# Optimization experiments

Measured on AMD Instinct MI355X. Metric: run time of the kernel, lower is better.

Reference implementation:

```python
import jax, jax.numpy as jnp
import numpy as np

DIM = 256; SEQ = 2048; WIN = 64; HEADS = 4; RANK = 32; LAYERS = 3; VOCAB = 32000
EPS = 1e-6

def _unit(v):
    # unit_normalize_values: project onto unit sphere along feature dim
    return v / jnp.maximum(jnp.linalg.norm(v, axis=-1, keepdims=True), EPS)

def _signed_softmax(s):
    # signed_softmax_state: sign(s) * softmax(|s|) over nodes
    return jnp.sign(s) * jax.nn.softmax(jnp.abs(s), axis=-1)

def setup_inputs() -> dict:
    key = jax.random.key(0)
    ks = jax.random.split(key, 10)
    d = DIM
    return {
        "input_ids": jax.random.randint(ks[0], (2, SEQ), 0, VOCAB, dtype=jnp.int32),
        "emb": 0.02 * jax.random.normal(ks[1], (VOCAB, d), jnp.float32),
        "pos_emb": 0.02 * jax.random.normal(ks[2], (SEQ, d), jnp.float32),
        "anchor_val": 0.02 * jax.random.normal(ks[3], (d,), jnp.float32),
        "anchor_state": jnp.zeros((), jnp.float32),
        "Ws": 0.02 * jax.random.normal(ks[4], (d,), jnp.float32),
        "bs": jnp.zeros((), jnp.float32),
        "U": 0.02 * jax.random.normal(ks[5], (LAYERS, d, HEADS, RANK), jnp.float32),
        "V": 0.02 * jax.random.normal(ks[6], (LAYERS, d, HEADS, RANK), jnp.float32),
        "W1": 0.02 * jax.random.normal(ks[7], (LAYERS, d, 2 * d), jnp.float32),
        "b1": jnp.zeros((LAYERS, 2 * d), jnp.float32),
        "W2": 0.02 * jax.random.normal(ks[8], (LAYERS, 2 * d, d), jnp.float32),
        "b2": jnp.zeros((LAYERS, d), jnp.float32),
    }

def _forward(emb, pos_emb, anchor_val, anchor_state, Ws, bs, U, V, W1, b1, W2, b2, input_ids):
    B, S = input_ids.shape
    tok = emb[input_ids] + pos_emb[None, :S]          # [B,S,D]
    state_src = tok                                    # state projected from pre-unit-norm values
    tok = _unit(tok)
    tstate = state_src @ Ws + bs                       # [B,S] scalar state per node
    val = jnp.concatenate([jnp.broadcast_to(_unit(anchor_val), (B, 1, DIM)), tok], axis=1)
    state = jnp.concatenate([jnp.broadcast_to(anchor_state, (B, 1)), tstate], axis=1)
    N = S + 1
    offs = jnp.arange(-WIN, WIN + 1)
    idx = jnp.arange(N)[:, None] + offs[None, :]       # [N,K]
    valid = (idx >= 0) & (idx < N)
    idxc = jnp.clip(idx, 0, N - 1)
    inv_sqrt_r = np.float32(1.0 / np.sqrt(RANK))
    for l in range(LAYERS):
        q = jnp.einsum('bnd,dhr->bnhr', val, U[l])
        k = jnp.einsum('bnd,dhr->bnhr', val, V[l])
        knb = k[:, idxc]                               # [B,N,K,H,R] window gather
        s = jnp.einsum('bnhr,bnkhr->bnkh', q, knb) * inv_sqrt_r
        s = s.max(axis=-1)                             # max head-aggregate [B,N,K]
        a = jnp.where(valid, jnp.abs(s), -jnp.inf)
        wgt = jnp.where(valid, jnp.sign(s) * jax.nn.softmax(a, axis=-1), 0.0)  # signed-abs-softmax edges
        dval = jnp.einsum('bnk,bnkd->bnd', wgt, val[:, idxc])
        dstate = jnp.sum(wgt * state[:, idxc], axis=-1)
        # apply_delta: residual + norm(identity) + unit-norm + touched-mask where
        updated = val + dval
        nv = _unit(updated)
        touched = jnp.max(jnp.abs(jax.lax.stop_gradient(dval)), axis=-1, keepdims=True) > 0
        val = jnp.where(touched, nv, updated)
        state = _signed_softmax(state + dstate)
        # residual feed-forward then re-unit-norm
        h = jax.nn.gelu(jnp.einsum('bnd,dh->bnh', val, W1[l]) + b1[l], approximate=False)
        val = _unit(val + jnp.einsum('bnh,hd->bnd', h, W2[l]) + b2[l])
    return state, val

def reference(input_ids, emb, pos_emb, anchor_val, anchor_state, Ws, bs, U, V, W1, b1, W2, b2):
    return _forward(emb, pos_emb, anchor_val, anchor_state, Ws, bs, U, V, W1, b1, W2, b2, input_ids)
```

## Files before the change

### kernel.cpp

```cpp
#include <hip/hip_runtime.h>
#include <hip/hip_bf16.h>
#include <math.h>

#define BB 2
#define SS 2048
#define NN 2049
#define MM (BB*NN)
#define DD 256
#define HR 128
#define NHEAD 4
#define WINW 64
#define DFF 512
#define EPSF 1e-6f
#define TB8 257

typedef __attribute__((ext_vector_type(8))) short bf16x8;
typedef __attribute__((ext_vector_type(4))) float f32x4;

__device__ __forceinline__ float wave_sum(float v) {
    v += __shfl_down(v, 32, 64); v += __shfl_down(v, 16, 64);
    v += __shfl_down(v, 8, 64);  v += __shfl_down(v, 4, 64);
    v += __shfl_down(v, 2, 64);  v += __shfl_down(v, 1, 64);
    return v;
}
__device__ __forceinline__ float wave_max(float v) {
    v = fmaxf(v, __shfl_down(v, 32, 64)); v = fmaxf(v, __shfl_down(v, 16, 64));
    v = fmaxf(v, __shfl_down(v, 8, 64));  v = fmaxf(v, __shfl_down(v, 4, 64));
    v = fmaxf(v, __shfl_down(v, 2, 64));  v = fmaxf(v, __shfl_down(v, 1, 64));
    return v;
}
__device__ __forceinline__ float block_sum(float v, float* red) {
    v = wave_sum(v);
    __syncthreads();
    if ((threadIdx.x & 63) == 0) red[threadIdx.x >> 6] = v;
    __syncthreads();
    return red[0] + red[1] + red[2] + red[3];
}
__device__ __forceinline__ float sgnf(float x) {
    return (x > 0.f) ? 1.f : ((x < 0.f) ? -1.f : 0.f);
}
__device__ __forceinline__ ushort f2b(float x) {
    __hip_bfloat16 h = __float2bfloat16(x);
    return *(ushort*)&h;
}
__device__ __forceinline__ float b2f(ushort u) {
    unsigned int v = ((unsigned int)u) << 16;
    return *(float*)&v;
}
__device__ __forceinline__ void split3(float x, ushort& h, ushort& m, ushort& l) {
    h = f2b(x);
    float r1 = x - b2f(h);
    m = f2b(r1);
    l = f2b(r1 - b2f(m));
}
__device__ __forceinline__ void pack_map(int e, int N, int& k, int& n) {
    int j = e & 7;
    int l = (e >> 3) & 63;
    int c = e >> 9;
    int ntiles = N >> 4;
    int kt = c / ntiles, nt = c - kt * ntiles;
    k = kt * 32 + ((l >> 4) << 3) + j;
    n = nt * 16 + (l & 15);
}

__global__ void pre_kernel(const int* __restrict__ ids,
                           const float* __restrict__ emb,
                           const float* __restrict__ pos,
                           const float* __restrict__ anchor_val,
                           const float* __restrict__ anchor_state,
                           const float* __restrict__ Ws,
                           const float* __restrict__ bs,
                           float* __restrict__ val,
                           float* __restrict__ state,
                           const float* __restrict__ W1, const float* __restrict__ W2,
                           const float* __restrict__ U,  const float* __restrict__ V,
                           ushort* __restrict__ W1ph, ushort* __restrict__ W1pl,
                           ushort* __restrict__ W2ph, ushort* __restrict__ W2pl,
                           ushort* __restrict__ U0, ushort* __restrict__ U1,
                           ushort* __restrict__ U2,
                           ushort* __restrict__ V0, ushort* __restrict__ V1,
                           ushort* __restrict__ V2) {
    __shared__ float red[4];
    int bid = blockIdx.x;
    int t = threadIdx.x;
    if (bid < MM) {
        int b = bid / NN, n = bid % NN;
        float e;
        if (n == 0) {
            e = anchor_val[t];
        } else {
            int id = ids[b * SS + (n - 1)];
            e = emb[(size_t)id * DD + t] + pos[(size_t)(n - 1) * DD + t];
        }
        float ss = block_sum(e * e, red);
        float ts = block_sum(e * Ws[t], red);
        float rn = 1.f / fmaxf(sqrtf(ss), EPSF);
        float o = e * rn;
        val[(size_t)bid * DD + t] = o;
        if (t == 0) state[bid] = (n == 0) ? anchor_state[0] : (ts + bs[0]);
        return;
    }
    int idx = (bid - MM) * 256 + t;
    int l = idx / 327680;
    int r = idx - l * 327680;
    if (l >= 3) return;
    int k, n;
    if (r < 131072) {
        int e = r;
        pack_map(e, 512, k, n);
        float s = W1[(size_t)l * 131072 + (size_t)k * 512 + n];
        ushort h = f2b(s);
        W1ph[(size_t)l * 131072 + e] = h;
        W1pl[(size_t)l * 131072 + e] = f2b(s - b2f(h));
    } else if (r < 262144) {
        int e = r - 131072;
        pack_map(e, 256, k, n);
        float s = W2[(size_t)l * 131072 + (size_t)k * 256 + n];
        ushort h = f2b(s);
        W2ph[(size_t)l * 131072 + e] = h;
        W2pl[(size_t)l * 131072 + e] = f2b(s - b2f(h));
    } else if (r < 294912) {
        int e = r - 262144;
        pack_map(e, 128, k, n);
        ushort h, m, lo;
        split3(U[(size_t)l * 32768 + (size_t)k * 128 + n], h, m, lo);
        U0[(size_t)l * 32768 + e] = h;
        U1[(size_t)l * 32768 + e] = m;
        U2[(size_t)l * 32768 + e] = lo;
    } else {
        int e = r - 294912;
        pack_map(e, 128, k, n);
        ushort h, m, lo;
        split3(V[(size_t)l * 32768 + (size_t)k * 128 + n], h, m, lo);
        V0[(size_t)l * 32768 + e] = h;
        V1[(size_t)l * 32768 + e] = m;
        V2[(size_t)l * 32768 + e] = lo;
    }
}

__global__ __launch_bounds__(256, 3)
void proj_kernel(const float* __restrict__ Xin,
                 const ushort* __restrict__ U0, const ushort* __restrict__ U1,
                 const ushort* __restrict__ U2,
                 const ushort* __restrict__ V0, const ushort* __restrict__ V1,
                 const ushort* __restrict__ V2,
                 ushort* __restrict__ q0, ushort* __restrict__ q1,
                 ushort* __restrict__ q2,
                 ushort* __restrict__ k0, ushort* __restrict__ k1,
                 ushort* __restrict__ k2,
                 float* __restrict__ valG, int donorm) {
    __shared__ __align__(16) ushort pln[3][16 * 256];
    int t = threadIdx.x;
    int w = t >> 6, l = t & 63;
    int lm = l & 15, quad = l >> 4;
    int m0 = blockIdx.x * 16;
    bool isQ = (blockIdx.y == 0);
    const ushort* P0 = isQ ? U0 : V0;
    const ushort* P1 = isQ ? U1 : V1;
    const ushort* P2 = isQ ? U2 : V2;

    #pragma unroll
    for (int rr = 0; rr < 4; rr++) {
        int row = w * 4 + rr;
        int tok = m0 + row; if (tok > MM - 1) tok = MM - 1;
        f32x4 x = *(const f32x4*)(Xin + (size_t)tok * DD + l * 4);
        if (donorm) {
            float s = x[0]*x[0] + x[1]*x[1] + x[2]*x[2] + x[3]*x[3];
            #pragma unroll
            for (int off = 1; off < 64; off <<= 1) s += __shfl_xor(s, off, 64);
            float rn = 1.f / fmaxf(sqrtf(s), EPSF);
            x[0] *= rn; x[1] *= rn; x[2] *= rn; x[3] *= rn;
            if (isQ) *(f32x4*)(valG + (size_t)tok * DD + l * 4) = x;
        }
        ushort4 h4, m4, l4;
        ushort hh, mm, ll;
        split3(x[0], hh, mm, ll); h4.x = hh; m4.x = mm; l4.x = ll;
        split3(x[1], hh, mm, ll); h4.y = hh; m4.y = mm; l4.y = ll;
        split3(x[2], hh, mm, ll); h4.z = hh; m4.z = mm; l4.z = ll;
        split3(x[3], hh, mm, ll); h4.w = hh; m4.w = mm; l4.w = ll;
        unsigned byte = ((unsigned)(row * 512 + l * 8)) ^ ((unsigned)((row & 7) << 4));
        *(ushort4*)((char*)&pln[0][0] + byte) = h4;
        *(ushort4*)((char*)&pln[1][0] + byte) = m4;
        *(ushort4*)((char*)&pln[2][0] + byte) = l4;
    }
    __syncthreads();

    f32x4 acc[2];
    acc[0] = (f32x4)(0.f); acc[1] = (f32x4)(0.f);
    #pragma unroll
    for (int kt = 0; kt < 8; kt++) {
        unsigned abyte = ((unsigned)(lm * 512 + kt * 64 + quad * 16)) ^
                         ((unsigned)((lm & 7) << 4));
        bf16x8 a0 = *(const bf16x8*)((char*)&pln[0][0] + abyte);
        bf16x8 a1 = *(const bf16x8*)((char*)&pln[1][0] + abyte);
        bf16x8 a2 = *(const bf16x8*)((char*)&pln[2][0] + abyte);
        #pragma unroll
        for (int jj = 0; jj < 2; jj++) {
            int ntl = w * 2 + jj;
            size_t off = ((size_t)(kt * 8 + ntl) * 64 + l) * 8;
            bf16x8 b0 = *(const bf16x8*)(P0 + off);
            bf16x8 b1 = *(const bf16x8*)(P1 + off);
            bf16x8 b2 = *(const bf16x8*)(P2 + off);
            acc[jj] = __builtin_amdgcn_mfma_f32_16x16x32_bf16(a0, b0, acc[jj], 0, 0, 0);
            acc[jj] = __builtin_amdgcn_mfma_f32_16x16x32_bf16(a0, b1, acc[jj], 0, 0, 0);
            acc[jj] = __builtin_amdgcn_mfma_f32_16x16x32_bf16(a1, b0, acc[jj], 0, 0, 0);
            acc[jj] = __builtin_amdgcn_mfma_f32_16x16x32_bf16(a1, b1, acc[jj], 0, 0, 0);
            acc[jj] = __builtin_amdgcn_mfma_f32_16x16x32_bf16(a0, b2, acc[jj], 0, 0, 0);
            acc[jj] = __builtin_amdgcn_mfma_f32_16x16x32_bf16(a2, b0, acc[jj], 0, 0, 0);
        }
    }
    ushort* o0 = isQ ? q0 : k0;
    ushort* o1 = isQ ? q1 : k1;
    ushort* o2 = isQ ? q2 : k2;
    #pragma unroll
    for (int jj = 0; jj < 2; jj++) {
        int n = (w * 2 + jj) * 16 + lm;
        #pragma unroll
        for (int r = 0; r < 4; r++) {
            int tok = m0 + quad * 4 + r;
            if (tok < MM) {
                ushort h, m, lo;
                split3(acc[jj][r], h, m, lo);
                size_t oi = (size_t)tok * HR + n;
                o0[oi] = h; o1[oi] = m; o2[oi] = lo;
            }
        }
    }
}

__global__ __launch_bounds__(256, 3)
void attn_kernel(const float* __restrict__ val_in,
                 const float* __restrict__ state_in,
                 const ushort* __restrict__ q0, const ushort* __restrict__ q1,
                 const ushort* __restrict__ q2,
                 const ushort* __restrict__ k0, const ushort* __restrict__ k1,
                 const ushort* __restrict__ k2,
                 float* __restrict__ val_out,
                 ushort* __restrict__ vbH, ushort* __restrict__ vbM,
                 float* __restrict__ dstate_out) {
    __shared__ float sc4[NHEAD][8][148];
    __shared__ float wgt2[144][12];
    __shared__ float redS[8][4];
    __shared__ float redM[8][4];

    int b = blockIdx.x / TB8;
    int n0 = (blockIdx.x % TB8) * 8;
    int t = threadIdx.x;
    int w = t >> 6, l = t & 63;
    int lm = l & 15, quad = l >> 4;

    {
        int qrow = n0 + (lm & 7);
        if (qrow > NN - 1) qrow = NN - 1;
        size_t qa = ((size_t)(b * NN + qrow)) * HR + w * 32 + quad * 8;
        bf16x8 a0 = *(const bf16x8*)(q0 + qa);
        bf16x8 a1 = *(const bf16x8*)(q1 + qa);
        bf16x8 a2 = *(const bf16x8*)(q2 + qa);
        #pragma unroll
        for (int jt = 0; jt < 9; jt++) {
            int j = n0 - 64 + jt * 16 + lm;
            j = (j < 0) ? 0 : ((j > NN - 1) ? NN - 1 : j);
            size_t ka = ((size_t)(b * NN + j)) * HR + w * 32 + quad * 8;
            bf16x8 kf0 = *(const bf16x8*)(k0 + ka);
            bf16x8 kf1 = *(const bf16x8*)(k1 + ka);
            bf16x8 kf2 = *(const bf16x8*)(k2 + ka);
            f32x4 acc = (f32x4)(0.f);
            acc = __builtin_amdgcn_mfma_f32_16x16x32_bf16(a0, kf0, acc, 0, 0, 0);
            acc = __builtin_amdgcn_mfma_f32_16x16x32_bf16(a0, kf1, acc, 0, 0, 0);
            acc = __builtin_amdgcn_mfma_f32_16x16x32_bf16(a1, kf0, acc, 0, 0, 0);
            acc = __builtin_amdgcn_mfma_f32_16x16x32_bf16(a1, kf1, acc, 0, 0, 0);
            acc = __builtin_amdgcn_mfma_f32_16x16x32_bf16(a0, kf2, acc, 0, 0, 0);
            acc = __builtin_amdgcn_mfma_f32_16x16x32_bf16(a2, kf0, acc, 0, 0, 0);
            if (quad < 2) {
                #pragma unroll
                for (int r = 0; r < 4; r++)
                    sc4[w][quad * 4 + r][jt * 16 + lm] = acc[r];
            }
        }
    }
    __syncthreads();

    {
        int m = t >> 5, p = t & 31;
        int n = n0 + m;
        bool tokv = (n < NN);
        float sv[5]; bool vv[5];
        float mx = -INFINITY;
        #pragma unroll
        for (int i = 0; i < 5; i++) {
            int tap = p + 32 * i;
            bool inb = (tap < 144);
            int tapc = inb ? tap : 0;
            int j = n0 - 64 + tapc;
            float s0 = sc4[0][m][tapc], s1 = sc4[1][m][tapc];
            float s2 = sc4[2][m][tapc], s3 = sc4[3][m][tapc];
            float s = fmaxf(fmaxf(s0, s1), fmaxf(s2, s3)) * 0.17677669529663687f;
            bool v = inb && tokv && (tap >= m) && (tap <= m + 128) && (j >= 0) && (j < NN);
            sv[i] = s; vv[i] = v;
            if (v) mx = fmaxf(mx, fabsf(s));
        }
        for (int off = 16; off > 0; off >>= 1) mx = fmaxf(mx, __shfl_xor(mx, off, 64));
        float ee[5];
        float sum = 0.f;
        #pragma unroll
        for (int i = 0; i < 5; i++) {
            ee[i] = vv[i] ? expf(fabsf(sv[i]) - mx) : 0.f;
            sum += ee[i];
        }
        for (int off = 16; off > 0; off >>= 1) sum += __shfl_xor(sum, off, 64);
        float inv = (sum > 0.f) ? 1.f / sum : 0.f;
        float ds = 0.f;
        #pragma unroll
        for (int i = 0; i < 5; i++) {
            int tap = p + 32 * i;
            if (tap < 144) {
                float wg = vv[i] ? sgnf(sv[i]) * ee[i] * inv : 0.f;
                wgt2[tap][m] = wg;
                if (vv[i]) ds += wg * state_in[b * NN + (n0 - 64 + tap)];
            }
        }
        for (int off = 16; off > 0; off >>= 1) ds += __shfl_xor(ds, off, 64);
        if (p == 0 && tokv) dstate_out[b * NN + n] = ds;
    }
    __syncthreads();

    {
        int d = (t >> 2) * 4;
        int tg = t & 3;
        int tok0 = tg * 2, tok1 = tg * 2 + 1;
        int jlo = (n0 >= 64) ? 0 : (64 - n0);
        int jhi = NN - 1 - n0 + 64; if (jhi > 135) jhi = 135;
        const float* vbase = val_in + ((size_t)(b * NN + n0 - 64)) * DD + d;
        f32x4 acc0 = (f32x4)(0.f), acc1 = (f32x4)(0.f);
        int jj = jlo;
        for (; jj + 3 <= jhi; jj += 4) {
            f32x4 v0 = *(const f32x4*)(vbase + (size_t)(jj + 0) * DD);
            f32x4 v1 = *(const f32x4*)(vbase + (size_t)(jj + 1) * DD);
            f32x4 v2 = *(const f32x4*)(vbase + (size_t)(jj + 2) * DD);
            f32x4 v3 = *(const f32x4*)(vbase + (size_t)(jj + 3) * DD);
            float wa0 = wgt2[jj + 0][tok0], wa1 = wgt2[jj + 0][tok1];
            float wb0 = wgt2[jj + 1][tok0], wb1 = wgt2[jj + 1][tok1];
            float wc0 = wgt2[jj + 2][tok0], wc1 = wgt2[jj + 2][tok1];
            float wd0 = wgt2[jj + 3][tok0], wd1 = wgt2[jj + 3][tok1];
            #pragma unroll
            for (int c = 0; c < 4; c++) {
                acc0[c] += v0[c] * wa0 + v1[c] * wb0 + v2[c] * wc0 + v3[c] * wd0;
                acc1[c] += v0[c] * wa1 + v1[c] * wb1 + v2[c] * wc1 + v3[c] * wd1;
            }
        }
        for (; jj <= jhi; jj++) {
            f32x4 v = *(const f32x4*)(vbase + (size_t)jj * DD);
            float w0 = wgt2[jj][tok0], w1 = wgt2[jj][tok1];
            #pragma unroll
            for (int c = 0; c < 4; c++) {
                acc0[c] += v[c] * w0;
                acc1[c] += v[c] * w1;
            }
        }
        f32x4 u[2]; f32x4 ac[2]; ac[0] = acc0; ac[1] = acc1;
        #pragma unroll
        for (int ti = 0; ti < 2; ti++) {
            int tok = tg * 2 + ti;
            int n = n0 + tok;
            f32x4 vold = (f32x4)(0.f);
            if (n < NN) vold = *(const f32x4*)(val_in + ((size_t)(b * NN + n)) * DD + d);
            u[ti] = vold + ac[ti];
            float s = u[ti][0]*u[ti][0] + u[ti][1]*u[ti][1] + u[ti][2]*u[ti][2] + u[ti][3]*u[ti][3];
            float mb = fmaxf(fmaxf(fabsf(ac[ti][0]), fabsf(ac[ti][1])),
                             fmaxf(fabsf(ac[ti][2]), fabsf(ac[ti][3])));
            for (int off = 4; off <= 32; off <<= 1) {
                s += __shfl_xor(s, off, 64);
                mb = fmaxf(mb, __shfl_xor(mb, off, 64));
            }
            if ((l >> 2) == 0) { redS[tok][w] = s; redM[tok][w] = mb; }
        }
        __syncthreads();
        #pragma unroll
        for (int ti = 0; ti < 2; ti++) {
            int tok = tg * 2 + ti;
            int n = n0 + tok;
            if (n < NN) {
                float ss = redS[tok][0] + redS[tok][1] + redS[tok][2] + redS[tok][3];
                float mab = fmaxf(fmaxf(redM[tok][0], redM[tok][1]),
                                  fmaxf(redM[tok][2], redM[tok][3]));
                float rn = 1.f / fmaxf(sqrtf(ss), EPSF);
                f32x4 o = u[ti];
                if (mab > 0.f) { o[0] *= rn; o[1] *= rn; o[2] *= rn; o[3] *= rn; }
                size_t oi = ((size_t)(b * NN + n)) * DD + d;
                *(f32x4*)(val_out + oi) = o;
                ushort4 hv, mv;
                {
                    ushort h0 = f2b(o[0]); hv.x = h0; mv.x = f2b(o[0] - b2f(h0));
                    ushort h1 = f2b(o[1]); hv.y = h1; mv.y = f2b(o[1] - b2f(h1));
                    ushort h2 = f2b(o[2]); hv.z = h2; mv.z = f2b(o[2] - b2f(h2));
                    ushort h3 = f2b(o[3]); hv.w = h3; mv.w = f2b(o[3] - b2f(h3));
                }
                *(ushort4*)(vbH + oi) = hv;
                *(ushort4*)(vbM + oi) = mv;
            }
        }
    }
}

__global__ __launch_bounds__(256, 3)
void ffn1_kernel(const ushort* __restrict__ XbH, const ushort* __restrict__ XbM,
                 const ushort* __restrict__ W1h, const ushort* __restrict__ W1l,
                 const float*  __restrict__ b1,
                 ushort* __restrict__ Hh, ushort* __restrict__ Hl,
                 const float* __restrict__ state_in, const float* __restrict__ dstate,
                 float* __restrict__ state_out) {
    __shared__ float red[8];
    int t = threadIdx.x;

    if (blockIdx.x == 257) {
        int b = blockIdx.y;
        float lmax = -INFINITY;
        for (int n = t; n < NN; n += 256) {
            float x = state_in[b * NN + n] + dstate[b * NN + n];
            lmax = fmaxf(lmax, fabsf(x));
        }
        lmax = wave_max(lmax);
        if ((t & 63) == 0) red[t >> 6] = lmax;
        __syncthreads();
        float m = fmaxf(fmaxf(red[0], red[1]), fmaxf(red[2], red[3]));
        float lsum = 0.f;
        for (int n = t; n < NN; n += 256)
            lsum += expf(fabsf(state_in[b * NN + n] + dstate[b * NN + n]) - m);
        lsum = wave_sum(lsum);
        __syncthreads();
        if ((t & 63) == 0) red[4 + (t >> 6)] = lsum;
        __syncthreads();
        float inv = 1.f / (red[4] + red[5] + red[6] + red[7]);
        for (int n = t; n < NN; n += 256) {
            float x = state_in[b * NN + n] + dstate[b * NN + n];
            state_out[b * NN + n] = sgnf(x) * expf(fabsf(x) - m) * inv;
        }
        return;
    }

    int w = t >> 6, l = t & 63;
    int lm = l & 15, quad = l >> 4;
    int m0 = blockIdx.x * 16;
    int nh = blockIdx.y;
    int row0 = m0 + lm; if (row0 > MM - 1) row0 = MM - 1;
    const ushort* xh = XbH + (size_t)row0 * DD + quad * 8;
    const ushort* xm = XbM + (size_t)row0 * DD + quad * 8;

    f32x4 acc[4];
    #pragma unroll
    for (int jj = 0; jj < 4; jj++) acc[jj] = (f32x4)(0.f);

    #pragma unroll
    for (int kt = 0; kt < 8; kt++) {
        bf16x8 ah = *(const bf16x8*)(xh + kt * 32);
        bf16x8 am = *(const bf16x8*)(xm + kt * 32);
        #pragma unroll
        for (int jj = 0; jj < 4; jj++) {
            int ntl = w * 4 + jj;
            size_t off = ((size_t)(kt * 32 + nh * 16 + ntl) * 64 + l) * 8;
            bf16x8 bh = *(const bf16x8*)(W1h + off);
            bf16x8 bl = *(const bf16x8*)(W1l + off);
            acc[jj] = __builtin_amdgcn_mfma_f32_16x16x32_bf16(ah, bh, acc[jj], 0, 0, 0);
            acc[jj] = __builtin_amdgcn_mfma_f32_16x16x32_bf16(am, bh, acc[jj], 0, 0, 0);
            acc[jj] = __builtin_amdgcn_mfma_f32_16x16x32_bf16(ah, bl, acc[jj], 0, 0, 0);
        }
    }
    #pragma unroll
    for (int jj = 0; jj < 4; jj++) {
        int gn = nh * 256 + (w * 4 + jj) * 16 + lm;
        float bb = b1[gn];
        #pragma unroll
        for (int r = 0; r < 4; r++) {
            int tok = m0 + quad * 4 + r;
            if (tok < MM) {
                float x = acc[jj][r] + bb;
                float g = 0.5f * x * (1.f + erff(x * 0.70710678118654752f));
                ushort gh = f2b(g);
                size_t oi = (size_t)tok * DFF + gn;
                Hh[oi] = gh;
                Hl[oi] = f2b(g - b2f(gh));
            }
        }
    }
}

__global__ __launch_bounds__(256, 4)
void ffn2_kernel(const ushort* __restrict__ Hh, const ushort* __restrict__ Hl,
                 const float*  __restrict__ Xf,
                 const ushort* __restrict__ W2h, const ushort* __restrict__ W2l,
                 const float*  __restrict__ b2,
                 float* __restrict__ Yb) {
    int t = threadIdx.x;
    int w = t >> 6, l = t & 63;
    int lm = l & 15, quad = l >> 4;
    int m0 = blockIdx.x * 16;
    int nh = blockIdx.y;
    int row0 = m0 + lm; if (row0 > MM - 1) row0 = MM - 1;
    const ushort* xh = Hh + (size_t)row0 * DFF + quad * 8;
    const ushort* xl = Hl + (size_t)row0 * DFF + quad * 8;

    f32x4 acc[2];
    acc[0] = (f32x4)(0.f); acc[1] = (f32x4)(0.f);

    #pragma unroll
    for (int kt = 0; kt < 16; kt++) {
        bf16x8 ah = *(const bf16x8*)(xh + kt * 32);
        bf16x8 al = *(const bf16x8*)(xl + kt * 32);
        #pragma unroll
        for (int jj = 0; jj < 2; jj++) {
            int ntl = w * 2 + jj;
            size_t off = ((size_t)(kt * 16 + nh * 8 + ntl) * 64 + l) * 8;
            bf16x8 bh = *(const bf16x8*)(W2h + off);
            bf16x8 bl = *(const bf16x8*)(W2l + off);
            acc[jj] = __builtin_amdgcn_mfma_f32_16x16x32_bf16(ah, bh, acc[jj], 0, 0, 0);
            acc[jj] = __builtin_amdgcn_mfma_f32_16x16x32_bf16(al, bh, acc[jj], 0, 0, 0);
            acc[jj] = __builtin_amdgcn_mfma_f32_16x16x32_bf16(ah, bl, acc[jj], 0, 0, 0);
        }
    }
    #pragma unroll
    for (int jj = 0; jj < 2; jj++) {
        int gn = nh * 128 + (w * 2 + jj) * 16 + lm;
        float bb = b2[gn];
        #pragma unroll
        for (int r = 0; r < 4; r++) {
            int tok = m0 + quad * 4 + r;
            if (tok < MM) {
                size_t oi = (size_t)tok * DD + gn;
                Yb[oi] = Xf[oi] + acc[jj][r] + bb;
            }
        }
    }
}

__global__ void ffn3f_kernel(const float* __restrict__ Yb,
                             float* __restrict__ val_out) {
    int t = threadIdx.x;
    int w = t >> 6, l = t & 63;
    int row = blockIdx.x * 4 + w;
    if (row >= MM) return;
    f32x4 y = *(const f32x4*)(Yb + (size_t)row * DD + l * 4);
    float s = y[0]*y[0] + y[1]*y[1] + y[2]*y[2] + y[3]*y[3];
    #pragma unroll
    for (int off = 1; off < 64; off <<= 1) s += __shfl_xor(s, off, 64);
    float rn = 1.f / fmaxf(sqrtf(s), EPSF);
    f32x4 o;
    o[0] = y[0] * rn; o[1] = y[1] * rn; o[2] = y[2] * rn; o[3] = y[3] * rn;
    *(f32x4*)(val_out + (size_t)row * DD + l * 4) = o;
}

extern "C" void kernel_launch(void* const* d_in, const int* in_sizes, int n_in,
                              void* d_out, int out_size, void* d_ws, size_t ws_size,
                              hipStream_t stream) {
    const int*   ids          = (const int*)d_in[0];
    const float* emb          = (const float*)d_in[1];
    const float* pos          = (const float*)d_in[2];
    const float* anchor_val   = (const float*)d_in[3];
    const float* anchor_state = (const float*)d_in[4];
    const float* Ws           = (const float*)d_in[5];
    const float* bs           = (const float*)d_in[6];
    const float* U            = (const float*)d_in[7];
    const float* V            = (const float*)d_in[8];
    const float* W1           = (const float*)d_in[9];
    const float* b1           = (const float*)d_in[10];
    const float* W2           = (const float*)d_in[11];
    const float* b2           = (const float*)d_in[12];
    float* out = (float*)d_out;

    ushort* p = (ushort*)d_ws;
    ushort* vB0 = p; p += (size_t)MM * DD;
    ushort* vB1 = p; p += (size_t)MM * DD;
    ushort* q0b = p; p += (size_t)MM * HR;
    ushort* q1b = p; p += (size_t)MM * HR;
    ushort* q2b = p; p += (size_t)MM * HR;
    ushort* k0b = p; p += (size_t)MM * HR;
    ushort* k1b = p; p += (size_t)MM * HR;
    ushort* k2b = p; p += (size_t)MM * HR;
    ushort* Hh  = p; p += (size_t)MM * DFF;
    ushort* Hl  = p; p += (size_t)MM * DFF;
    ushort* W1ph = p; p += 3 * 131072;
    ushort* W1pl = p; p += 3 * 131072;
    ushort* W2ph = p; p += 3 * 131072;
    ushort* W2pl = p; p += 3 * 131072;
    ushort* U0p = p; p += 3 * 32768;
    ushort* U1p = p; p += 3 * 32768;
    ushort* U2p = p; p += 3 * 32768;
    ushort* V0p = p; p += 3 * 32768;
    ushort* V1p = p; p += 3 * 32768;
    ushort* V2p = p; p += 3 * 32768;
    float* f = (float*)p;
    float* valA = f; f += (size_t)MM * DD;
    float* valB = f; f += (size_t)MM * DD;
    float* Yb   = f; f += (size_t)MM * DD;
    float* st0  = f; f += MM;
    float* st1  = f; f += MM;
    float* dst  = f; f += MM;

    pre_kernel<<<MM + 3840, 256, 0, stream>>>(ids, emb, pos, anchor_val, anchor_state,
                                              Ws, bs, valA, st0,
                                              W1, W2, U, V,
                                              W1ph, W1pl, W2ph, W2pl,
                                              U0p, U1p, U2p, V0p, V1p, V2p);
    float* s_in = st0;
    float* s_out = st1;
    for (int l = 0; l < 3; l++) {
        const float* Xin = (l == 0) ? valA : Yb;
        proj_kernel<<<dim3(257, 2), 256, 0, stream>>>(
            Xin,
            U0p + (size_t)l * 32768, U1p + (size_t)l * 32768, U2p + (size_t)l * 32768,
            V0p + (size_t)l * 32768, V1p + (size_t)l * 32768, V2p + (size_t)l * 32768,
            q0b, q1b, q2b, k0b, k1b, k2b,
            valA, (l == 0) ? 0 : 1);
        attn_kernel<<<BB * TB8, 256, 0, stream>>>(valA, s_in,
                                                  q0b, q1b, q2b, k0b, k1b, k2b,
                                                  valB, vB0, vB1, dst);
        ffn1_kernel<<<dim3(258, 2), 256, 0, stream>>>(
            vB0, vB1,
            W1ph + (size_t)l * 131072, W1pl + (size_t)l * 131072, b1 + (size_t)l * DFF,
            Hh, Hl,
            s_in, dst, (l == 2) ? out : s_out);
        ffn2_kernel<<<dim3(257, 2), 256, 0, stream>>>(
            Hh, Hl, valB,
            W2ph + (size_t)l * 131072, W2pl + (size_t)l * 131072, b2 + (size_t)l * DD,
            Yb);
        float* tmp = s_in; s_in = s_out; s_out = tmp;
    }
    ffn3f_kernel<<<(MM + 3) / 4, 256, 0, stream>>>(Yb, out + MM);
}
```

Before: 360.0 us.

## Fuse FFN1, FFN2, unit-norm and next-layer QK projection into one kernel

Replaces the per-layer ffn1, ffn2, final-normalize and next-layer projection kernels with one fused kernel. Each 16-row block keeps the GELU hidden activations and the residual output in shared memory instead of round-tripping through global H and Y buffers. The same block then normalizes the rows and computes the next layer's q/k split-bf16 projections. This cuts launches and global traffic, but the grid shrinks from about 516 blocks to 259, each doing all 512 FFN columns with more registers, and occupancy bound drops to 2, which may reduce parallelism.

```diff
diff --git a/kernel.cpp b/kernel.cpp
--- a/kernel.cpp
+++ b/kernel.cpp
@@ -9,7 +9,6 @@
 #define DD 256
 #define HR 128
 #define NHEAD 4
-#define WINW 64
 #define DFF 512
 #define EPSF 1e-6f
 #define TB8 257
@@ -63,44 +62,36 @@
     n = nt * 16 + (l & 15);
 }
 
-__global__ void pre_kernel(const int* __restrict__ ids,
-                           const float* __restrict__ emb,
-                           const float* __restrict__ pos,
-                           const float* __restrict__ anchor_val,
-                           const float* __restrict__ anchor_state,
-                           const float* __restrict__ Ws,
-                           const float* __restrict__ bs,
-                           float* __restrict__ val,
-                           float* __restrict__ state,
-                           const float* __restrict__ W1, const float* __restrict__ W2,
-                           const float* __restrict__ U,  const float* __restrict__ V,
-                           ushort* __restrict__ W1ph, ushort* __restrict__ W1pl,
-                           ushort* __restrict__ W2ph, ushort* __restrict__ W2pl,
-                           ushort* __restrict__ U0, ushort* __restrict__ U1,
-                           ushort* __restrict__ U2,
-                           ushort* __restrict__ V0, ushort* __restrict__ V1,
-                           ushort* __restrict__ V2) {
-    __shared__ float red[4];
-    int bid = blockIdx.x;
-    int t = threadIdx.x;
-    if (bid < MM) {
-        int b = bid / NN, n = bid % NN;
-        float e;
-        if (n == 0) {
-            e = anchor_val[t];
-        } else {
-            int id = ids[b * SS + (n - 1)];
-            e = emb[(size_t)id * DD + t] + pos[(size_t)(n - 1) * DD + t];
-        }
-        float ss = block_sum(e * e, red);
-        float ts = block_sum(e * Ws[t], red);
-        float rn = 1.f / fmaxf(sqrtf(ss), EPSF);
-        float o = e * rn;
-        val[(size_t)bid * DD + t] = o;
-        if (t == 0) state[bid] = (n == 0) ? anchor_state[0] : (ts + bs[0]);
-        return;
-    }
-    int idx = (bid - MM) * 256 + t;
+
+__device__ __forceinline__ void embed_job(int row, int t, float* red,
+    const int* __restrict__ ids, const float* __restrict__ emb,
+    const float* __restrict__ pos, const float* __restrict__ anchor_val,
+    const float* __restrict__ anchor_state, const float* __restrict__ Ws,
+    const float* __restrict__ bs, float* __restrict__ val, float* __restrict__ state)
+{
+    int b = row / NN, n = row % NN;
+    float e;
+    if (n == 0) {
+        e = anchor_val[t];
+    } else {
+        int id = ids[b * SS + (n - 1)];
+        e = emb[(size_t)id * DD + t] + pos[(size_t)(n - 1) * DD + t];
+    }
+    float ss = block_sum(e * e, red);
+    float ts = block_sum(e * Ws[t], red);
+    float rn = 1.f / fmaxf(sqrtf(ss), EPSF);
+    val[(size_t)row * DD + t] = e * rn;
+    if (t == 0) state[row] = (n == 0) ? anchor_state[0] : (ts + bs[0]);
+}
+
+__device__ __forceinline__ void pack_job(int idx,
+    const float* __restrict__ W1, const float* __restrict__ W2,
+    const float* __restrict__ U,  const float* __restrict__ V,
+    ushort* __restrict__ W1ph, ushort* __restrict__ W1pl,
+    ushort* __restrict__ W2ph, ushort* __restrict__ W2pl,
+    ushort* __restrict__ U0, ushort* __restrict__ U1, ushort* __restrict__ U2,
+    ushort* __restrict__ V0, ushort* __restrict__ V1, ushort* __restrict__ V2)
+{
     int l = idx / 327680;
     int r = idx - l * 327680;
     if (l >= 3) return;
@@ -138,6 +129,56 @@
     }
 }
 
+__device__ __forceinline__ void state_job(int b, int t, float* red,
+    const float* __restrict__ state_in, const float* __restrict__ dstate,
+    float* __restrict__ state_out)
+{
+    float lmax = -INFINITY;
+    for (int n = t; n < NN; n += 256) {
+        float x = state_in[b * NN + n] + dstate[b * NN + n];
+        lmax = fmaxf(lmax, fabsf(x));
+    }
+    lmax = wave_max(lmax);
+    if ((t & 63) == 0) red[t >> 6] = lmax;
+    __syncthreads();
+    float m = fmaxf(fmaxf(red[0], red[1]), fmaxf(red[2], red[3]));
+    float lsum = 0.f;
+    for (int n = t; n < NN; n += 256)
+        lsum += expf(fabsf(state_in[b * NN + n] + dstate[b * NN + n]) - m);
+    lsum = wave_sum(lsum);
+    __syncthreads();
+    if ((t & 63) == 0) red[4 + (t >> 6)] = lsum;
+    __syncthreads();
+    float inv = 1.f / (red[4] + red[5] + red[6] + red[7]);
+    for (int n = t; n < NN; n += 256) {
+        float x = state_in[b * NN + n] + dstate[b * NN + n];
+        state_out[b * NN + n] = sgnf(x) * expf(fabsf(x) - m) * inv;
+    }
+}
+
+
+__global__ void pre_kernel(const int* __restrict__ ids, const float* __restrict__ emb,
+                           const float* __restrict__ pos, const float* __restrict__ anchor_val,
+                           const float* __restrict__ anchor_state, const float* __restrict__ Ws,
+                           const float* __restrict__ bs, float* __restrict__ val,
+                           float* __restrict__ state,
+                           const float* __restrict__ W1, const float* __restrict__ W2,
+                           const float* __restrict__ U,  const float* __restrict__ V,
+                           ushort* W1ph, ushort* W1pl, ushort* W2ph, ushort* W2pl,
+                           ushort* U0, ushort* U1, ushort* U2,
+                           ushort* V0, ushort* V1, ushort* V2) {
+    __shared__ float red[4];
+    int bid = blockIdx.x;
+    int t = threadIdx.x;
+    if (bid < MM) {
+        embed_job(bid, t, red, ids, emb, pos, anchor_val, anchor_state, Ws, bs, val, state);
+        return;
+    }
+    pack_job((bid - MM) * 256 + t, W1, W2, U, V,
+             W1ph, W1pl, W2ph, W2pl, U0, U1, U2, V0, V1, V2);
+}
+
+
 __global__ __launch_bounds__(256, 3)
 void proj_kernel(const float* __restrict__ Xin,
                  const ushort* __restrict__ U0, const ushort* __restrict__ U1,
@@ -147,9 +188,8 @@
                  ushort* __restrict__ q0, ushort* __restrict__ q1,
                  ushort* __restrict__ q2,
                  ushort* __restrict__ k0, ushort* __restrict__ k1,
-                 ushort* __restrict__ k2,
-                 float* __restrict__ valG, int donorm) {
-    __shared__ __align__(16) ushort pln[3][16 * 256];
+                 ushort* __restrict__ k2) {
+    __shared__ __align__(16) char smem[24576];
     int t = threadIdx.x;
     int w = t >> 6, l = t & 63;
     int lm = l & 15, quad = l >> 4;
@@ -164,14 +204,6 @@
         int row = w * 4 + rr;
         int tok = m0 + row; if (tok > MM - 1) tok = MM - 1;
         f32x4 x = *(const f32x4*)(Xin + (size_t)tok * DD + l * 4);
-        if (donorm) {
-            float s = x[0]*x[0] + x[1]*x[1] + x[2]*x[2] + x[3]*x[3];
-            #pragma unroll
-            for (int off = 1; off < 64; off <<= 1) s += __shfl_xor(s, off, 64);
-            float rn = 1.f / fmaxf(sqrtf(s), EPSF);
-            x[0] *= rn; x[1] *= rn; x[2] *= rn; x[3] *= rn;
-            if (isQ) *(f32x4*)(valG + (size_t)tok * DD + l * 4) = x;
-        }
         ushort4 h4, m4, l4;
         ushort hh, mm, ll;
         split3(x[0], hh, mm, ll); h4.x = hh; m4.x = mm; l4.x = ll;
@@ -179,9 +211,9 @@
         split3(x[2], hh, mm, ll); h4.z = hh; m4.z = mm; l4.z = ll;
         split3(x[3], hh, mm, ll); h4.w = hh; m4.w = mm; l4.w = ll;
         unsigned byte = ((unsigned)(row * 512 + l * 8)) ^ ((unsigned)((row & 7) << 4));
-        *(ushort4*)((char*)&pln[0][0] + byte) = h4;
-        *(ushort4*)((char*)&pln[1][0] + byte) = m4;
-        *(ushort4*)((char*)&pln[2][0] + byte) = l4;
+        *(ushort4*)(smem + 0 * 8192 + byte) = h4;
+        *(ushort4*)(smem + 1 * 8192 + byte) = m4;
+        *(ushort4*)(smem + 2 * 8192 + byte) = l4;
     }
     __syncthreads();
 
@@ -191,9 +223,9 @@
     for (int kt = 0; kt < 8; kt++) {
         unsigned abyte = ((unsigned)(lm * 512 + kt * 64 + quad * 16)) ^
                          ((unsigned)((lm & 7) << 4));
-        bf16x8 a0 = *(const bf16x8*)((char*)&pln[0][0] + abyte);
-        bf16x8 a1 = *(const bf16x8*)((char*)&pln[1][0] + abyte);
-        bf16x8 a2 = *(const bf16x8*)((char*)&pln[2][0] + abyte);
+        bf16x8 a0 = *(const bf16x8*)(smem + 0 * 8192 + abyte);
+        bf16x8 a1 = *(const bf16x8*)(smem + 1 * 8192 + abyte);
+        bf16x8 a2 = *(const bf16x8*)(smem + 2 * 8192 + abyte);
         #pragma unroll
         for (int jj = 0; jj < 2; jj++) {
             int ntl = w * 2 + jj;
@@ -227,6 +259,7 @@
         }
     }
 }
+
 
 __global__ __launch_bounds__(256, 3)
 void attn_kernel(const float* __restrict__ val_in,
@@ -402,151 +435,216 @@
     }
 }
 
-__global__ __launch_bounds__(256, 3)
-void ffn1_kernel(const ushort* __restrict__ XbH, const ushort* __restrict__ XbM,
-                 const ushort* __restrict__ W1h, const ushort* __restrict__ W1l,
-                 const float*  __restrict__ b1,
-                 ushort* __restrict__ Hh, ushort* __restrict__ Hl,
-                 const float* __restrict__ state_in, const float* __restrict__ dstate,
-                 float* __restrict__ state_out) {
-    __shared__ float red[8];
+
+__global__ __launch_bounds__(256, 2)
+void fusedF_kernel(const ushort* __restrict__ vb0, const ushort* __restrict__ vb1,
+                   const float*  __restrict__ valB,
+                   const ushort* __restrict__ W1h, const ushort* __restrict__ W1l,
+                   const float*  __restrict__ b1,
+                   const ushort* __restrict__ W2h, const ushort* __restrict__ W2l,
+                   const float*  __restrict__ b2,
+                   const ushort* __restrict__ U0, const ushort* __restrict__ U1,
+                   const ushort* __restrict__ U2,
+                   const ushort* __restrict__ V0, const ushort* __restrict__ V1,
+                   const ushort* __restrict__ V2,
+                   ushort* __restrict__ q0, ushort* __restrict__ q1,
+                   ushort* __restrict__ q2,
+                   ushort* __restrict__ k0, ushort* __restrict__ k1,
+                   ushort* __restrict__ k2,
+                   float* __restrict__ valA,
+                   const float* __restrict__ s_in, const float* __restrict__ dstate,
+                   float* __restrict__ s_out,
+                   float* __restrict__ out2, int last)
+{
+    __shared__ __align__(16) char smem[49152];
     int t = threadIdx.x;
-
-    if (blockIdx.x == 257) {
-        int b = blockIdx.y;
-        float lmax = -INFINITY;
-        for (int n = t; n < NN; n += 256) {
-            float x = state_in[b * NN + n] + dstate[b * NN + n];
-            lmax = fmaxf(lmax, fabsf(x));
-        }
-        lmax = wave_max(lmax);
-        if ((t & 63) == 0) red[t >> 6] = lmax;
-        __syncthreads();
-        float m = fmaxf(fmaxf(red[0], red[1]), fmaxf(red[2], red[3]));
-        float lsum = 0.f;
-        for (int n = t; n < NN; n += 256)
-            lsum += expf(fabsf(state_in[b * NN + n] + dstate[b * NN + n]) - m);
-        lsum = wave_sum(lsum);
-        __syncthreads();
-        if ((t & 63) == 0) red[4 + (t >> 6)] = lsum;
-        __syncthreads();
-        float inv = 1.f / (red[4] + red[5] + red[6] + red[7]);
-        for (int n = t; n < NN; n += 256) {
-            float x = state_in[b * NN + n] + dstate[b * NN + n];
-            state_out[b * NN + n] = sgnf(x) * expf(fabsf(x) - m) * inv;
-        }
+    int bid = blockIdx.x;
+
+    if (bid >= 257) {
+        if (bid - 257 < BB) state_job(bid - 257, t, (float*)smem, s_in, dstate, s_out);
         return;
     }
 
     int w = t >> 6, l = t & 63;
     int lm = l & 15, quad = l >> 4;
-    int m0 = blockIdx.x * 16;
-    int nh = blockIdx.y;
+    int m0 = bid * 16;
     int row0 = m0 + lm; if (row0 > MM - 1) row0 = MM - 1;
-    const ushort* xh = XbH + (size_t)row0 * DD + quad * 8;
-    const ushort* xm = XbM + (size_t)row0 * DD + quad * 8;
-
-    f32x4 acc[4];
-    #pragma unroll
-    for (int jj = 0; jj < 4; jj++) acc[jj] = (f32x4)(0.f);
-
-    #pragma unroll
-    for (int kt = 0; kt < 8; kt++) {
-        bf16x8 ah = *(const bf16x8*)(xh + kt * 32);
-        bf16x8 am = *(const bf16x8*)(xm + kt * 32);
-        #pragma unroll
-        for (int jj = 0; jj < 4; jj++) {
-            int ntl = w * 4 + jj;
-            size_t off = ((size_t)(kt * 32 + nh * 16 + ntl) * 64 + l) * 8;
-            bf16x8 bh = *(const bf16x8*)(W1h + off);
-            bf16x8 bl = *(const bf16x8*)(W1l + off);
-            acc[jj] = __builtin_amdgcn_mfma_f32_16x16x32_bf16(ah, bh, acc[jj], 0, 0, 0);
-            acc[jj] = __builtin_amdgcn_mfma_f32_16x16x32_bf16(am, bh, acc[jj], 0, 0, 0);
-            acc[jj] = __builtin_amdgcn_mfma_f32_16x16x32_bf16(ah, bl, acc[jj], 0, 0, 0);
-        }
-    }
-    #pragma unroll
-    for (int jj = 0; jj < 4; jj++) {
-        int gn = nh * 256 + (w * 4 + jj) * 16 + lm;
-        float bb = b1[gn];
-        #pragma unroll
-        for (int r = 0; r < 4; r++) {
-            int tok = m0 + quad * 4 + r;
-            if (tok < MM) {
+
+    {
+        const ushort* xh = vb0 + (size_t)row0 * DD + quad * 8;
+        const ushort* xm = vb1 + (size_t)row0 * DD + quad * 8;
+        f32x4 acc[8];
+        #pragma unroll
+        for (int jj = 0; jj < 8; jj++) acc[jj] = (f32x4)(0.f);
+        #pragma unroll
+        for (int kt = 0; kt < 8; kt++) {
+            bf16x8 ah = *(const bf16x8*)(xh + kt * 32);
+            bf16x8 am = *(const bf16x8*)(xm + kt * 32);
+            #pragma unroll
+            for (int jj = 0; jj < 8; jj++) {
+                int nt = w * 8 + jj;
+                size_t off = ((size_t)(kt * 32 + nt) * 64 + l) * 8;
+                bf16x8 bh = *(const bf16x8*)(W1h + off);
+                bf16x8 bl = *(const bf16x8*)(W1l + off);
+                acc[jj] = __builtin_amdgcn_mfma_f32_16x16x32_bf16(ah, bh, acc[jj], 0, 0, 0);
+                acc[jj] = __builtin_amdgcn_mfma_f32_16x16x32_bf16(am, bh, acc[jj], 0, 0, 0);
+                acc[jj] = __builtin_amdgcn_mfma_f32_16x16x32_bf16(ah, bl, acc[jj], 0, 0, 0);
+            }
+        }
+        #pragma unroll
+        for (int jj = 0; jj < 8; jj++) {
+            int gn = (w * 8 + jj) * 16 + lm;
+            float bb = b1[gn];
+            #pragma unroll
+            for (int r = 0; r < 4; r++) {
+                int rho = quad * 4 + r;
                 float x = acc[jj][r] + bb;
                 float g = 0.5f * x * (1.f + erff(x * 0.70710678118654752f));
                 ushort gh = f2b(g);
-                size_t oi = (size_t)tok * DFF + gn;
-                Hh[oi] = gh;
-                Hl[oi] = f2b(g - b2f(gh));
-            }
-        }
-    }
-}
-
-__global__ __launch_bounds__(256, 4)
-void ffn2_kernel(const ushort* __restrict__ Hh, const ushort* __restrict__ Hl,
-                 const float*  __restrict__ Xf,
-                 const ushort* __restrict__ W2h, const ushort* __restrict__ W2l,
-                 const float*  __restrict__ b2,
-                 float* __restrict__ Yb) {
-    int t = threadIdx.x;
-    int w = t >> 6, l = t & 63;
-    int lm = l & 15, quad = l >> 4;
-    int m0 = blockIdx.x * 16;
-    int nh = blockIdx.y;
-    int row0 = m0 + lm; if (row0 > MM - 1) row0 = MM - 1;
-    const ushort* xh = Hh + (size_t)row0 * DFF + quad * 8;
-    const ushort* xl = Hl + (size_t)row0 * DFF + quad * 8;
-
-    f32x4 acc[2];
-    acc[0] = (f32x4)(0.f); acc[1] = (f32x4)(0.f);
+                unsigned byte = ((unsigned)(rho * 1024 + gn * 2)) ^
+                                ((unsigned)((rho & 7) << 4));
+                *(ushort*)(smem + byte) = gh;
+                *(ushort*)(smem + 16384 + byte) = f2b(g - b2f(gh));
+            }
+        }
+    }
+    __syncthreads();
+
+    {
+        f32x4 acc[4];
+        #pragma unroll
+        for (int jj = 0; jj < 4; jj++) acc[jj] = (f32x4)(0.f);
+        #pragma unroll
+        for (int kt = 0; kt < 16; kt++) {
+            unsigned ab = ((unsigned)(lm * 1024 + kt * 64 + quad * 16)) ^
+                          ((unsigned)((lm & 7) << 4));
+            bf16x8 ah = *(const bf16x8*)(smem + ab);
+            bf16x8 al = *(const bf16x8*)(smem + 16384 + ab);
+            #pragma unroll
+            for (int jj = 0; jj < 4; jj++) {
+                int nt = w * 4 + jj;
+                size_t off = ((size_t)(kt * 16 + nt) * 64 + l) * 8;
+                bf16x8 bh = *(const bf16x8*)(W2h + off);
+                bf16x8 bl = *(const bf16x8*)(W2l + off);
+                acc[jj] = __builtin_amdgcn_mfma_f32_16x16x32_bf16(ah, bh, acc[jj], 0, 0, 0);
+                acc[jj] = __builtin_amdgcn_mfma_f32_16x16x32_bf16(al, bh, acc[jj], 0, 0, 0);
+                acc[jj] = __builtin_amdgcn_mfma_f32_16x16x32_bf16(ah, bl, acc[jj], 0, 0, 0);
+            }
+        }
+        #pragma unroll
+        for (int jj = 0; jj < 4; jj++) {
+            int gn = (w * 4 + jj) * 16 + lm;
+            float bb = b2[gn];
+            #pragma unroll
+            for (int r = 0; r < 4; r++) {
+                int rho = quad * 4 + r;
+                int tok = m0 + rho;
+                float y = 0.f;
+                if (tok < MM) y = valB[(size_t)tok * DD + gn] + acc[jj][r] + bb;
+                unsigned byte = ((unsigned)(rho * 1024 + gn * 4)) ^
+                                ((unsigned)((rho & 7) << 4));
+                *(float*)(smem + 32768 + byte) = y;
+            }
+        }
+    }
+    __syncthreads();
+
+    if (last) {
+        #pragma unroll
+        for (int rr = 0; rr < 4; rr++) {
+            int row = w * 4 + rr;
+            int tok = m0 + row;
+            unsigned byte = ((unsigned)(row * 1024 + l * 16)) ^
+                            ((unsigned)((row & 7) << 4));
+            f32x4 y = *(const f32x4*)(smem + 32768 + byte);
+            float s = y[0]*y[0] + y[1]*y[1] + y[2]*y[2] + y[3]*y[3];
+            #pragma unroll
+            for (int off = 1; off < 64; off <<= 1) s += __shfl_xor(s, off, 64);
+            float rn = 1.f / fmaxf(sqrtf(s), EPSF);
+            if (tok < MM) {
+                f32x4 o;
+                o[0] = y[0] * rn; o[1] = y[1] * rn; o[2] = y[2] * rn; o[3] = y[3] * rn;
+                *(f32x4*)(out2 + (size_t)tok * DD + l * 4) = o;
+            }
+        }
+        return;
+    }
 
     #pragma unroll
-    for (int kt = 0; kt < 16; kt++) {
-        bf16x8 ah = *(const bf16x8*)(xh + kt * 32);
-        bf16x8 al = *(const bf16x8*)(xl + kt * 32);
+    for (int rr = 0; rr < 4; rr++) {
+        int row = w * 4 + rr;
+        int tok = m0 + row;
+        unsigned ybyte = ((unsigned)(row * 1024 + l * 16)) ^
+                         ((unsigned)((row & 7) << 4));
+        f32x4 x = *(const f32x4*)(smem + 32768 + ybyte);
+        float s = x[0]*x[0] + x[1]*x[1] + x[2]*x[2] + x[3]*x[3];
+        #pragma unroll
+        for (int off = 1; off < 64; off <<= 1) s += __shfl_xor(s, off, 64);
+        float rn = 1.f / fmaxf(sqrtf(s), EPSF);
+        x[0] *= rn; x[1] *= rn; x[2] *= rn; x[3] *= rn;
+        if (tok < MM) *(f32x4*)(valA + (size_t)tok * DD + l * 4) = x;
+        ushort4 h4, m4, l4;
+        ushort hh, mm, ll;
+        split3(x[0], hh, mm, ll); h4.x = hh; m4.x = mm; l4.x = ll;
+        split3(x[1], hh, mm, ll); h4.y = hh; m4.y = mm; l4.y = ll;
+        split3(x[2], hh, mm, ll); h4.z = hh; m4.z = mm; l4.z = ll;
+        split3(x[3], hh, mm, ll); h4.w = hh; m4.w = mm; l4.w = ll;
+        unsigned pbyte = ((unsigned)(row * 512 + l * 8)) ^ ((unsigned)((row & 7) << 4));
+        *(ushort4*)(smem + 0 * 8192 + pbyte) = h4;
+        *(ushort4*)(smem + 1 * 8192 + pbyte) = m4;
+        *(ushort4*)(smem + 2 * 8192 + pbyte) = l4;
+    }
+    __syncthreads();
+
+    #pragma unroll 1
+    for (int pass = 0; pass < 2; pass++) {
+        const ushort* P0 = pass ? V0 : U0;
+        const ushort* P1 = pass ? V1 : U1;
+        const ushort* P2 = pass ? V2 : U2;
+        ushort* o0 = pass ? k0 : q0;
+        ushort* o1 = pass ? k1 : q1;
+        ushort* o2 = pass ? k2 : q2;
+        f32x4 acc[2];
+        acc[0] = (f32x4)(0.f); acc[1] = (f32x4)(0.f);
+        #pragma unroll
+        for (int kt = 0; kt < 8; kt++) {
+            unsigned abyte = ((unsigned)(lm * 512 + kt * 64 + quad * 16)) ^
+                             ((unsigned)((lm & 7) << 4));
+            bf16x8 a0 = *(const bf16x8*)(smem + 0 * 8192 + abyte);
+            bf16x8 a1 = *(const bf16x8*)(smem + 1 * 8192 + abyte);
+            bf16x8 a2 = *(const bf16x8*)(smem + 2 * 8192 + abyte);
+            #pragma unroll
+            for (int jj = 0; jj < 2; jj++) {
+                int ntl = w * 2 + jj;
+                size_t off = ((size_t)(kt * 8 + ntl) * 64 + l) * 8;
+                bf16x8 b0 = *(const bf16x8*)(P0 + off);
+                bf16x8 b1 = *(const bf16x8*)(P1 + off);
+                bf16x8 b2 = *(const bf16x8*)(P2 + off);
+                acc[jj] = __builtin_amdgcn_mfma_f32_16x16x32_bf16(a0, b0, acc[jj], 0, 0, 0);
+                acc[jj] = __builtin_amdgcn_mfma_f32_16x16x32_bf16(a0, b1, acc[jj], 0, 0, 0);
+                acc[jj] = __builtin_amdgcn_mfma_f32_16x16x32_bf16(a1, b0, acc[jj], 0, 0, 0);
+                acc[jj] = __builtin_amdgcn_mfma_f32_16x16x32_bf16(a1, b1, acc[jj], 0, 0, 0);
+                acc[jj] = __builtin_amdgcn_mfma_f32_16x16x32_bf16(a0, b2, acc[jj], 0, 0, 0);
+                acc[jj] = __builtin_amdgcn_mfma_f32_16x16x32_bf16(a2, b0, acc[jj], 0, 0, 0);
+            }
+        }
         #pragma unroll
         for (int jj = 0; jj < 2; jj++) {
-            int ntl = w * 2 + jj;
-            size_t off = ((size_t)(kt * 16 + nh * 8 + ntl) * 64 + l) * 8;
-            bf16x8 bh = *(const bf16x8*)(W2h + off);
-            bf16x8 bl = *(const bf16x8*)(W2l + off);
-            acc[jj] = __builtin_amdgcn_mfma_f32_16x16x32_bf16(ah, bh, acc[jj], 0, 0, 0);
-            acc[jj] = __builtin_amdgcn_mfma_f32_16x16x32_bf16(al, bh, acc[jj], 0, 0, 0);
-            acc[jj] = __builtin_amdgcn_mfma_f32_16x16x32_bf16(ah, bl, acc[jj], 0, 0, 0);
-        }
-    }
-    #pragma unroll
-    for (int jj = 0; jj < 2; jj++) {
-        int gn = nh * 128 + (w * 2 + jj) * 16 + lm;
-        float bb = b2[gn];
-        #pragma unroll
-        for (int r = 0; r < 4; r++) {
-            int tok = m0 + quad * 4 + r;
-            if (tok < MM) {
-                size_t oi = (size_t)tok * DD + gn;
-                Yb[oi] = Xf[oi] + acc[jj][r] + bb;
-            }
-        }
-    }
-}
-
-__global__ void ffn3f_kernel(const float* __restrict__ Yb,
-                             float* __restrict__ val_out) {
-    int t = threadIdx.x;
-    int w = t >> 6, l = t & 63;
-    int row = blockIdx.x * 4 + w;
-    if (row >= MM) return;
-    f32x4 y = *(const f32x4*)(Yb + (size_t)row * DD + l * 4);
-    float s = y[0]*y[0] + y[1]*y[1] + y[2]*y[2] + y[3]*y[3];
-    #pragma unroll
-    for (int off = 1; off < 64; off <<= 1) s += __shfl_xor(s, off, 64);
-    float rn = 1.f / fmaxf(sqrtf(s), EPSF);
-    f32x4 o;
-    o[0] = y[0] * rn; o[1] = y[1] * rn; o[2] = y[2] * rn; o[3] = y[3] * rn;
-    *(f32x4*)(val_out + (size_t)row * DD + l * 4) = o;
-}
+            int n = (w * 2 + jj) * 16 + lm;
+            #pragma unroll
+            for (int r = 0; r < 4; r++) {
+                int tok = m0 + quad * 4 + r;
+                if (tok < MM) {
+                    ushort h, m, lo;
+                    split3(acc[jj][r], h, m, lo);
+                    size_t oi = (size_t)tok * HR + n;
+                    o0[oi] = h; o1[oi] = m; o2[oi] = lo;
+                }
+            }
+        }
+    }
+}
+
 
 extern "C" void kernel_launch(void* const* d_in, const int* in_sizes, int n_in,
                               void* d_out, int out_size, void* d_ws, size_t ws_size,
@@ -575,8 +673,6 @@
     ushort* k0b = p; p += (size_t)MM * HR;
     ushort* k1b = p; p += (size_t)MM * HR;
     ushort* k2b = p; p += (size_t)MM * HR;
-    ushort* Hh  = p; p += (size_t)MM * DFF;
-    ushort* Hl  = p; p += (size_t)MM * DFF;
     ushort* W1ph = p; p += 3 * 131072;
     ushort* W1pl = p; p += 3 * 131072;
     ushort* W2ph = p; p += 3 * 131072;
@@ -590,7 +686,6 @@
     float* f = (float*)p;
     float* valA = f; f += (size_t)MM * DD;
     float* valB = f; f += (size_t)MM * DD;
-    float* Yb   = f; f += (size_t)MM * DD;
     float* st0  = f; f += MM;
     float* st1  = f; f += MM;
     float* dst  = f; f += MM;
@@ -600,29 +695,27 @@
                                               W1, W2, U, V,
                                               W1ph, W1pl, W2ph, W2pl,
                                               U0p, U1p, U2p, V0p, V1p, V2p);
+    proj_kernel<<<dim3(257, 2), 256, 0, stream>>>(
+        valA, U0p, U1p, U2p, V0p, V1p, V2p,
+        q0b, q1b, q2b, k0b, k1b, k2b);
+
     float* s_in = st0;
     float* s_out = st1;
     for (int l = 0; l < 3; l++) {
-        const float* Xin = (l == 0) ? valA : Yb;
-        proj_kernel<<<dim3(257, 2), 256, 0, stream>>>(
-            Xin,
-            U0p + (size_t)l * 32768, U1p + (size_t)l * 32768, U2p + (size_t)l * 32768,
-            V0p + (size_t)l * 32768, V1p + (size_t)l * 32768, V2p + (size_t)l * 32768,
-            q0b, q1b, q2b, k0b, k1b, k2b,
-            valA, (l == 0) ? 0 : 1);
         attn_kernel<<<BB * TB8, 256, 0, stream>>>(valA, s_in,
                                                   q0b, q1b, q2b, k0b, k1b, k2b,
                                                   valB, vB0, vB1, dst);
-        ffn1_kernel<<<dim3(258, 2), 256, 0, stream>>>(
-            vB0, vB1,
+        int ln = (l < 2) ? (l + 1) : 0;
+        fusedF_kernel<<<259, 256, 0, stream>>>(
+            vB0, vB1, valB,
             W1ph + (size_t)l * 131072, W1pl + (size_t)l * 131072, b1 + (size_t)l * DFF,
-            Hh, Hl,
-            s_in, dst, (l == 2) ? out : s_out);
-        ffn2_kernel<<<dim3(257, 2), 256, 0, stream>>>(
-            Hh, Hl, valB,
             W2ph + (size_t)l * 131072, W2pl + (size_t)l * 131072, b2 + (size_t)l * DD,
-            Yb);
+            U0p + (size_t)ln * 32768, U1p + (size_t)ln * 32768, U2p + (size_t)ln * 32768,
+            V0p + (size_t)ln * 32768, V1p + (size_t)ln * 32768, V2p + (size_t)ln * 32768,
+            q0b, q1b, q2b, k0b, k1b, k2b,
+            valA,
+            s_in, dst, (l == 2) ? out : s_out,
+            out + MM, (l == 2) ? 1 : 0);
         float* tmp = s_in; s_in = s_out; s_out = tmp;
     }
-    ffn3f_kernel<<<(MM + 3) / 4, 256, 0, stream>>>(Yb, out + MM);
-}
+}
```

Result: faster. 344.3 us (-4.4%).
